# Optimization experiments

Measured on AMD Instinct MI355X. Metric: run time of the kernel, lower is better.

## Reference

```python
import jax, jax.numpy as jnp
import numpy as np

LAMBDA = 0.95   # fast-weight decay
ETA = 0.5       # Hebbian write rate
EPS = 1e-5      # LayerNorm epsilon
S_LOOP = 2      # inner read steps


def setup_inputs() -> dict:
    key = jax.random.key(0)
    ks = jax.random.split(key, 3)
    T, B, d_g, d_h = 32, 32, 256, 512
    z_seq = jax.random.normal(ks[0], (T, B, d_g), dtype=jnp.float32)
    # kaiming-uniform-ish / xavier-ish scaled weights
    W_h = jax.random.normal(ks[1], (d_h, d_h), dtype=jnp.float32) * (2.0 / d_h) ** 0.5
    W_g = jax.random.normal(ks[2], (d_h, d_g), dtype=jnp.float32) * (2.0 / (d_h + d_g)) ** 0.5
    b_h = jnp.zeros((d_h,), jnp.float32)
    ln_gamma = jnp.ones((d_h,), jnp.float32)
    ln_beta = jnp.zeros((d_h,), jnp.float32)
    return {"z_seq": z_seq, "W_h": W_h, "W_g": W_g, "b_h": b_h,
            "ln_gamma": ln_gamma, "ln_beta": ln_beta}


def reference(z_seq, W_h, W_g, b_h, ln_gamma, ln_beta):
    T, B, _ = z_seq.shape
    d_h = W_h.shape[0]

    def ln(x):
        mu = jnp.mean(x, axis=-1, keepdims=True)
        var = jnp.mean((x - mu) ** 2, axis=-1, keepdims=True)
        return (x - mu) * jax.lax.rsqrt(var + EPS) * ln_gamma + ln_beta

    def inner_read(h_base, A):
        # h = relu(LN(h_base)); then S fast-weight reads h <- relu(LN(h_base + A h))
        h = jax.nn.relu(ln(h_base))
        for _ in range(S_LOOP):
            Ah = jnp.einsum('bij,bj->bi', A, h)  # [B, d_h]
            h = jax.nn.relu(ln(h_base + Ah))
        return h

    def step(carry, z_t):
        h, A = carry
        h_base = h @ W_h.T + z_t @ W_g.T + b_h  # [B, d_h]
        h = inner_read(h_base, A)
        # Hebbian outer-product write: A <- lambda*A + eta * h h^T
        A = LAMBDA * A + ETA * jnp.einsum('bi,bj->bij', h, h)
        return (h, A), None

    h0 = jnp.zeros((B, d_h), z_seq.dtype)
    A0 = jnp.zeros((B, d_h, d_h), z_seq.dtype)
    (h, A), _ = jax.lax.scan(step, (h0, A0), z_seq[:-1])

    # last step: read-only (no A update)
    h_base = h @ W_h.T + z_seq[-1] @ W_g.T + b_h
    h = inner_read(h_base, A)
    return h
```

## Files before the change

### kernel.cpp

```cpp
#include <hip/hip_runtime.h>

typedef __attribute__((ext_vector_type(8))) short short8;
typedef __attribute__((ext_vector_type(4))) float f32x4;

constexpr int T_STEPS = 32;
constexpr int BATCH   = 32;
constexpr int DG      = 256;
constexpr int DH      = 512;
constexpr int NHIST   = 31;
constexpr int LDH     = 520;
constexpr int LDT     = 40;
constexpr float LAMBDA_ = 0.95f;
constexpr float ETA_    = 0.5f;
constexpr float EPS_    = 1e-5f;

__device__ __forceinline__ uint bf16cvt(float f) {
  uint u = __float_as_uint(f);
  return (u + 0x7FFFu + ((u >> 16) & 1u)) >> 16;
}
__device__ __forceinline__ uint pack2(float a, float b) {
  return bf16cvt(a) | (bf16cvt(b) << 16);
}

__global__ __launch_bounds__(512) void pack_kernel(
    const float* __restrict__ Wh, uint4* __restrict__ Wp) {
  const int f  = blockIdx.x * 512 + threadIdx.x;
  const int lf = f & 63;
  const int kk = (f >> 6) & 15;
  const int mt = f >> 10;
  const int r  = mt * 16 + (lf & 15);
  const int k0 = kk * 32 + (lf >> 4) * 8;
  const float4 a = *reinterpret_cast<const float4*>(Wh + (size_t)r * DH + k0);
  const float4 b = *reinterpret_cast<const float4*>(Wh + (size_t)r * DH + k0 + 4);
  Wp[f] = make_uint4(pack2(a.x, a.y), pack2(a.z, a.w),
                     pack2(b.x, b.y), pack2(b.z, b.w));
}

__global__ __launch_bounds__(512, 2) void rnn_kernel(
    const uint4* __restrict__ Wp, const float* __restrict__ z,
    const float* __restrict__ Wg, const float* __restrict__ bh,
    const float* __restrict__ g, const float* __restrict__ be,
    float* __restrict__ ZGg, float* __restrict__ out) {
  __shared__ uint4  stage[8][2][4][64];
  __shared__ ushort hist_bf[NHIST][LDH];
  __shared__ ushort histT[DH][LDT];
  __shared__ float  part[DH];
  __shared__ float  h_s[DH];
  __shared__ ushort hbf[DH];
  __shared__ float  red1[8], red2[8];
  __shared__ float  cc[NHIST + 1];
  __shared__ float  lam_pow[NHIST];

  const int tid  = threadIdx.x;
  const int lane = tid & 63;
  const int wave = tid >> 6;
  const int c    = lane & 15;
  const int gq   = lane >> 4;
  const int b    = blockIdx.x;
  const int r    = tid;

  if (tid == 0) {
    float p = 1.f;
    for (int k = 0; k < NHIST; ++k) { lam_pow[k] = p; p *= LAMBDA_; }
  }
  if (tid < NHIST + 1) cc[tid] = 0.f;
  {
    uint4 zz = make_uint4(0u, 0u, 0u, 0u);
#pragma unroll
    for (int i = 0; i < 5; ++i)
      reinterpret_cast<uint4*>(&histT[r][0])[i] = zz;
  }

  auto STAGE = [&](int kk, int slot) {
#pragma unroll
    for (int mt4 = 0; mt4 < 4; ++mt4) {
      const uint4* gsrc = Wp + (size_t)((wave * 4 + mt4) * 16 + kk) * 64 + lane;
      __builtin_amdgcn_global_load_lds(
          (const __attribute__((address_space(1))) uint*)gsrc,
          (__attribute__((address_space(3))) uint*)&stage[wave][slot][mt4][0],
          16, 0, 0);
    }
  };

#pragma unroll
  for (int mt4 = 0; mt4 < 4; ++mt4) {
    const int mt = wave * 4 + mt4;
    f32x4 acc0 = {0.f,0.f,0.f,0.f}, acc1 = {0.f,0.f,0.f,0.f};
#pragma unroll
    for (int kk = 0; kk < 8; ++kk) {
      const int k0 = kk * 32 + gq * 8;
      const float4 a  = *reinterpret_cast<const float4*>(Wg + (size_t)(mt*16 + c) * DG + k0);
      const float4 a2 = *reinterpret_cast<const float4*>(Wg + (size_t)(mt*16 + c) * DG + k0 + 4);
      const uint4 afu = make_uint4(pack2(a.x,a.y), pack2(a.z,a.w),
                                   pack2(a2.x,a2.y), pack2(a2.z,a2.w));
      const float* zb0 = z + ((size_t)c        * BATCH + b) * DG + k0;
      const float* zb1 = z + ((size_t)(16 + c) * BATCH + b) * DG + k0;
      const float4 b00 = *reinterpret_cast<const float4*>(zb0);
      const float4 b01 = *reinterpret_cast<const float4*>(zb0 + 4);
      const float4 b10 = *reinterpret_cast<const float4*>(zb1);
      const float4 b11 = *reinterpret_cast<const float4*>(zb1 + 4);
      const uint4 bf0 = make_uint4(pack2(b00.x,b00.y), pack2(b00.z,b00.w),
                                   pack2(b01.x,b01.y), pack2(b01.z,b01.w));
      const uint4 bf1 = make_uint4(pack2(b10.x,b10.y), pack2(b10.z,b10.w),
                                   pack2(b11.x,b11.y), pack2(b11.z,b11.w));
      acc0 = __builtin_amdgcn_mfma_f32_16x16x32_bf16(
          __builtin_bit_cast(short8, afu), __builtin_bit_cast(short8, bf0), acc0, 0,0,0);
      acc1 = __builtin_amdgcn_mfma_f32_16x16x32_bf16(
          __builtin_bit_cast(short8, afu), __builtin_bit_cast(short8, bf1), acc1, 0,0,0);
    }
    *reinterpret_cast<f32x4*>(&ZGg[((size_t)c        * BATCH + b) * DH + mt*16 + gq*4]) = acc0;
    *reinterpret_cast<f32x4*>(&ZGg[((size_t)(16 + c) * BATCH + b) * DH + mt*16 + gq*4]) = acc1;
  }
  __syncthreads();

  const float bh_r = bh[r], g_r = g[r], be_r = be[r];

  auto ln = [&](float x) -> float {
    float s1 = x, s2 = x * x;
#pragma unroll
    for (int off = 32; off; off >>= 1) {
      s1 += __shfl_xor(s1, off, 64);
      s2 += __shfl_xor(s2, off, 64);
    }
    if (lane == 0) { red1[wave] = s1; red2[wave] = s2; }
    __syncthreads();
    float a = 0.f, q = 0.f;
#pragma unroll
    for (int w2 = 0; w2 < 8; ++w2) { a += red1[w2]; q += red2[w2]; }
    const float mu = a * (1.f / DH);
    const float rs = rsqrtf(q * (1.f / DH) - mu * mu + EPS_);
    const float hv2 = fmaxf((x - mu) * rs * g_r + be_r, 0.f);
    h_s[r] = hv2;
    hbf[r] = (ushort)bf16cvt(hv2);
    __syncthreads();
    return hv2;
  };

  float hv = 0.f;
  for (int t = 0; t < T_STEPS; ++t) {
    float xb;
    if (t == 0) {
      xb = ZGg[(size_t)b * DH + r] + bh_r;
    } else {
      const float zgv = ZGg[((size_t)t * BATCH + b) * DH + r];
      asm volatile("s_waitcnt vmcnt(0)" ::: "memory");
      __builtin_amdgcn_sched_barrier(0);

      STAGE(0, 0);
      STAGE(1, 1);
      f32x4 acc[4] = {{0.f,0.f,0.f,0.f},{0.f,0.f,0.f,0.f},
                      {0.f,0.f,0.f,0.f},{0.f,0.f,0.f,0.f}};
#pragma unroll
      for (int kk = 0; kk < 16; ++kk) {
        const int slot = kk & 1;
        if (kk < 15) { asm volatile("s_waitcnt vmcnt(4)" ::: "memory"); }
        else         { asm volatile("s_waitcnt vmcnt(0)" ::: "memory"); }
        __builtin_amdgcn_sched_barrier(0);
        const uint4 a0 = stage[wave][slot][0][lane];
        const uint4 a1 = stage[wave][slot][1][lane];
        const uint4 a2 = stage[wave][slot][2][lane];
        const uint4 a3 = stage[wave][slot][3][lane];
        uint4 bvu = {0u,0u,0u,0u};
        if (c == 0)
          bvu = *reinterpret_cast<const uint4*>(&hbf[kk*32 + gq*8]);
        const short8 bv = __builtin_bit_cast(short8, bvu);
        acc[0] = __builtin_amdgcn_mfma_f32_16x16x32_bf16(
            __builtin_bit_cast(short8, a0), bv, acc[0], 0,0,0);
        acc[1] = __builtin_amdgcn_mfma_f32_16x16x32_bf16(
            __builtin_bit_cast(short8, a1), bv, acc[1], 0,0,0);
        acc[2] = __builtin_amdgcn_mfma_f32_16x16x32_bf16(
            __builtin_bit_cast(short8, a2), bv, acc[2], 0,0,0);
        acc[3] = __builtin_amdgcn_mfma_f32_16x16x32_bf16(
            __builtin_bit_cast(short8, a3), bv, acc[3], 0,0,0);
        if (kk < 14) STAGE(kk + 2, slot);
      }
      if (c == 0) {
#pragma unroll
        for (int mt4 = 0; mt4 < 4; ++mt4)
          *reinterpret_cast<f32x4*>(&part[(wave*4 + mt4)*16 + gq*4]) = acc[mt4];
      }
      __syncthreads();
      xb = part[r] + zgv + bh_r;
    }

    hv = ln(xb);

    if (t > 0) {
      for (int s = 0; s < 2; ++s) {
        const float4 c0 = *reinterpret_cast<const float4*>(&h_s[lane * 8]);
        const float4 c1 = *reinterpret_cast<const float4*>(&h_s[lane * 8 + 4]);
        for (int sp = wave; sp < t; sp += 8) {
          const uint4 hw = *reinterpret_cast<const uint4*>(&hist_bf[sp][lane * 8]);
          float d;
          d =      __uint_as_float(hw.x << 16)          * c0.x;
          d = fmaf(__uint_as_float(hw.x & 0xFFFF0000u), c0.y, d);
          d = fmaf(__uint_as_float(hw.y << 16),         c0.z, d);
          d = fmaf(__uint_as_float(hw.y & 0xFFFF0000u), c0.w, d);
          d = fmaf(__uint_as_float(hw.z << 16),         c1.x, d);
          d = fmaf(__uint_as_float(hw.z & 0xFFFF0000u), c1.y, d);
          d = fmaf(__uint_as_float(hw.w << 16),         c1.z, d);
          d = fmaf(__uint_as_float(hw.w & 0xFFFF0000u), c1.w, d);
#pragma unroll
          for (int off = 32; off; off >>= 1) d += __shfl_xor(d, off, 64);
          if (lane == 0) cc[sp] = ETA_ * lam_pow[t - 1 - sp] * d;
        }
        __syncthreads();
        float ah = 0.f;
#pragma unroll
        for (int q8 = 0; q8 < 4; ++q8) {
          const uint4 hw = *reinterpret_cast<const uint4*>(&histT[r][q8 * 8]);
          const uint w0 = hw.x, w1 = hw.y, w2 = hw.z, w3 = hw.w;
          ah = fmaf(cc[q8*8+0], __uint_as_float(w0 << 16),          ah);
          ah = fmaf(cc[q8*8+1], __uint_as_float(w0 & 0xFFFF0000u),  ah);
          ah = fmaf(cc[q8*8+2], __uint_as_float(w1 << 16),          ah);
          ah = fmaf(cc[q8*8+3], __uint_as_float(w1 & 0xFFFF0000u),  ah);
          ah = fmaf(cc[q8*8+4], __uint_as_float(w2 << 16),          ah);
          ah = fmaf(cc[q8*8+5], __uint_as_float(w2 & 0xFFFF0000u),  ah);
          ah = fmaf(cc[q8*8+6], __uint_as_float(w3 << 16),          ah);
          ah = fmaf(cc[q8*8+7], __uint_as_float(w3 & 0xFFFF0000u),  ah);
        }
        hv = ln(xb + ah);
      }
    }

    if (t < T_STEPS - 1) {
      const ushort hb16 = (ushort)bf16cvt(hv);
      hist_bf[t][r] = hb16;
      histT[r][t]   = hb16;
    }
  }

  out[(size_t)b * DH + r] = hv;
}

extern "C" void kernel_launch(void* const* d_in, const int* in_sizes, int n_in,
                              void* d_out, int out_size, void* d_ws, size_t ws_size,
                              hipStream_t stream) {
  const float* z     = (const float*)d_in[0];
  const float* W_h   = (const float*)d_in[1];
  const float* W_g   = (const float*)d_in[2];
  const float* b_h   = (const float*)d_in[3];
  const float* gamma = (const float*)d_in[4];
  const float* beta  = (const float*)d_in[5];
  float* out = (float*)d_out;

  float* ZGg = (float*)d_ws;
  uint4* Wp  = (uint4*)((char*)d_ws + (size_t)T_STEPS * BATCH * DH * 4);

  pack_kernel<<<dim3(64), dim3(512), 0, stream>>>(W_h, Wp);
  rnn_kernel<<<dim3(BATCH), dim3(512), 0, stream>>>(Wp, z, W_g, b_h,
                                                    gamma, beta, ZGg, out);
}
```

Measured before the change: 307.9 us.

## Compute fast-weight history dots with MFMA, keep ZG projection in LDS

Stores the Hebbian history in a single MFMA fragment layout in LDS. The history-times-h dot products now run as bf16 MFMAs with a cross-wave partial reduction, replacing per-wave shuffle reductions over two separate history copies. The precomputed input projection stays in LDS as bf16 instead of making a global round trip. The next step's W_h staging is prefetched across the step boundary, and __syncthreads is replaced by a lighter lgkmcnt-only barrier. In exchange the input projection loses precision to bf16, and the barrier no longer waits for outstanding global loads.

```diff
diff --git a/kernel.cpp b/kernel.cpp
--- a/kernel.cpp
+++ b/kernel.cpp
@@ -8,8 +8,6 @@
 constexpr int DG      = 256;
 constexpr int DH      = 512;
 constexpr int NHIST   = 31;
-constexpr int LDH     = 520;
-constexpr int LDT     = 40;
 constexpr float LAMBDA_ = 0.95f;
 constexpr float ETA_    = 0.5f;
 constexpr float EPS_    = 1e-5f;
@@ -20,6 +18,16 @@
 }
 __device__ __forceinline__ uint pack2(float a, float b) {
   return bf16cvt(a) | (bf16cvt(b) << 16);
+}
+__device__ __forceinline__ float bf2f(ushort u) {
+  return __uint_as_float(((uint)u) << 16);
+}
+
+__device__ __forceinline__ void block_barrier() {
+  __builtin_amdgcn_sched_barrier(0);
+  asm volatile("s_waitcnt lgkmcnt(0)" ::: "memory");
+  __builtin_amdgcn_s_barrier();
+  __builtin_amdgcn_sched_barrier(0);
 }
 
 __global__ __launch_bounds__(512) void pack_kernel(
@@ -40,15 +48,16 @@
     const uint4* __restrict__ Wp, const float* __restrict__ z,
     const float* __restrict__ Wg, const float* __restrict__ bh,
     const float* __restrict__ g, const float* __restrict__ be,
-    float* __restrict__ ZGg, float* __restrict__ out) {
+    float* __restrict__ out) {
   __shared__ uint4  stage[8][2][4][64];
-  __shared__ ushort hist_bf[NHIST][LDH];
-  __shared__ ushort histT[DH][LDT];
+  __shared__ uint4  hist_frag[2 * 16 * 64];
+  __shared__ ushort zg_bf[T_STEPS][DH];
   __shared__ float  part[DH];
   __shared__ float  h_s[DH];
   __shared__ ushort hbf[DH];
+  __shared__ float  pdots[8][32];
   __shared__ float  red1[8], red2[8];
-  __shared__ float  cc[NHIST + 1];
+  __shared__ float  cc[32];
   __shared__ float  lam_pow[NHIST];
 
   const int tid  = threadIdx.x;
@@ -63,13 +72,8 @@
     float p = 1.f;
     for (int k = 0; k < NHIST; ++k) { lam_pow[k] = p; p *= LAMBDA_; }
   }
-  if (tid < NHIST + 1) cc[tid] = 0.f;
-  {
-    uint4 zz = make_uint4(0u, 0u, 0u, 0u);
-#pragma unroll
-    for (int i = 0; i < 5; ++i)
-      reinterpret_cast<uint4*>(&histT[r][0])[i] = zz;
-  }
+  for (int i = tid; i < 2 * 16 * 64; i += 512)
+    hist_frag[i] = make_uint4(0u, 0u, 0u, 0u);
 
   auto STAGE = [&](int kk, int slot) {
 #pragma unroll
@@ -108,12 +112,15 @@
       acc1 = __builtin_amdgcn_mfma_f32_16x16x32_bf16(
           __builtin_bit_cast(short8, afu), __builtin_bit_cast(short8, bf1), acc1, 0,0,0);
     }
-    *reinterpret_cast<f32x4*>(&ZGg[((size_t)c        * BATCH + b) * DH + mt*16 + gq*4]) = acc0;
-    *reinterpret_cast<f32x4*>(&ZGg[((size_t)(16 + c) * BATCH + b) * DH + mt*16 + gq*4]) = acc1;
+    *reinterpret_cast<uint2*>(&zg_bf[c][mt*16 + gq*4]) =
+        make_uint2(pack2(acc0.x, acc0.y), pack2(acc0.z, acc0.w));
+    *reinterpret_cast<uint2*>(&zg_bf[16 + c][mt*16 + gq*4]) =
+        make_uint2(pack2(acc1.x, acc1.y), pack2(acc1.z, acc1.w));
   }
-  __syncthreads();
-
   const float bh_r = bh[r], g_r = g[r], be_r = be[r];
+  block_barrier();
+
+  STAGE(0, 0); STAGE(1, 1);
 
   auto ln = [&](float x) -> float {
     float s1 = x, s2 = x * x;
@@ -123,7 +130,7 @@
       s2 += __shfl_xor(s2, off, 64);
     }
     if (lane == 0) { red1[wave] = s1; red2[wave] = s2; }
-    __syncthreads();
+    block_barrier();
     float a = 0.f, q = 0.f;
 #pragma unroll
     for (int w2 = 0; w2 < 8; ++w2) { a += red1[w2]; q += red2[w2]; }
@@ -132,7 +139,7 @@
     const float hv2 = fmaxf((x - mu) * rs * g_r + be_r, 0.f);
     h_s[r] = hv2;
     hbf[r] = (ushort)bf16cvt(hv2);
-    __syncthreads();
+    block_barrier();
     return hv2;
   };
 
@@ -140,14 +147,8 @@
   for (int t = 0; t < T_STEPS; ++t) {
     float xb;
     if (t == 0) {
-      xb = ZGg[(size_t)b * DH + r] + bh_r;
+      xb = bf2f(zg_bf[0][r]) + bh_r;
     } else {
-      const float zgv = ZGg[((size_t)t * BATCH + b) * DH + r];
-      asm volatile("s_waitcnt vmcnt(0)" ::: "memory");
-      __builtin_amdgcn_sched_barrier(0);
-
-      STAGE(0, 0);
-      STAGE(1, 1);
       f32x4 acc[4] = {{0.f,0.f,0.f,0.f},{0.f,0.f,0.f,0.f},
                       {0.f,0.f,0.f,0.f},{0.f,0.f,0.f,0.f}};
 #pragma unroll
@@ -174,59 +175,66 @@
             __builtin_bit_cast(short8, a3), bv, acc[3], 0,0,0);
         if (kk < 14) STAGE(kk + 2, slot);
       }
+      if (t < T_STEPS - 1) { STAGE(0, 0); STAGE(1, 1); }
       if (c == 0) {
 #pragma unroll
         for (int mt4 = 0; mt4 < 4; ++mt4)
           *reinterpret_cast<f32x4*>(&part[(wave*4 + mt4)*16 + gq*4]) = acc[mt4];
       }
-      __syncthreads();
-      xb = part[r] + zgv + bh_r;
+      block_barrier();
+      xb = part[r] + bf2f(zg_bf[t][r]) + bh_r;
     }
 
     hv = ln(xb);
 
     if (t > 0) {
       for (int s = 0; s < 2; ++s) {
-        const float4 c0 = *reinterpret_cast<const float4*>(&h_s[lane * 8]);
-        const float4 c1 = *reinterpret_cast<const float4*>(&h_s[lane * 8 + 4]);
-        for (int sp = wave; sp < t; sp += 8) {
-          const uint4 hw = *reinterpret_cast<const uint4*>(&hist_bf[sp][lane * 8]);
-          float d;
-          d =      __uint_as_float(hw.x << 16)          * c0.x;
-          d = fmaf(__uint_as_float(hw.x & 0xFFFF0000u), c0.y, d);
-          d = fmaf(__uint_as_float(hw.y << 16),         c0.z, d);
-          d = fmaf(__uint_as_float(hw.y & 0xFFFF0000u), c0.w, d);
-          d = fmaf(__uint_as_float(hw.z << 16),         c1.x, d);
-          d = fmaf(__uint_as_float(hw.z & 0xFFFF0000u), c1.y, d);
-          d = fmaf(__uint_as_float(hw.w << 16),         c1.z, d);
-          d = fmaf(__uint_as_float(hw.w & 0xFFFF0000u), c1.w, d);
-#pragma unroll
-          for (int off = 32; off; off >>= 1) d += __shfl_xor(d, off, 64);
-          if (lane == 0) cc[sp] = ETA_ * lam_pow[t - 1 - sp] * d;
-        }
-        __syncthreads();
+        const int kk0 = 2 * wave, kk1 = kk0 + 1;
+        uint4 b0u = {0u,0u,0u,0u}, b1u = {0u,0u,0u,0u};
+        if (c == 0) {
+          b0u = *reinterpret_cast<const uint4*>(&hbf[kk0*32 + gq*8]);
+          b1u = *reinterpret_cast<const uint4*>(&hbf[kk1*32 + gq*8]);
+        }
+        const short8 b0 = __builtin_bit_cast(short8, b0u);
+        const short8 b1 = __builtin_bit_cast(short8, b1u);
+        f32x4 d0 = {0.f,0.f,0.f,0.f}, d1 = {0.f,0.f,0.f,0.f};
+        d0 = __builtin_amdgcn_mfma_f32_16x16x32_bf16(
+            __builtin_bit_cast(short8, hist_frag[kk0*64 + lane]), b0, d0, 0,0,0);
+        d0 = __builtin_amdgcn_mfma_f32_16x16x32_bf16(
+            __builtin_bit_cast(short8, hist_frag[kk1*64 + lane]), b1, d0, 0,0,0);
+        d1 = __builtin_amdgcn_mfma_f32_16x16x32_bf16(
+            __builtin_bit_cast(short8, hist_frag[(16+kk0)*64 + lane]), b0, d1, 0,0,0);
+        d1 = __builtin_amdgcn_mfma_f32_16x16x32_bf16(
+            __builtin_bit_cast(short8, hist_frag[(16+kk1)*64 + lane]), b1, d1, 0,0,0);
+        if (c == 0) {
+          *reinterpret_cast<f32x4*>(&pdots[wave][gq*4])      = d0;
+          *reinterpret_cast<f32x4*>(&pdots[wave][16 + gq*4]) = d1;
+        }
+        block_barrier();
+        if (tid < 32) {
+          float d = 0.f;
+#pragma unroll
+          for (int w = 0; w < 8; ++w) d += pdots[w][tid];
+          cc[tid] = (tid < t) ? ETA_ * lam_pow[t - 1 - tid] * d : 0.f;
+        }
+        block_barrier();
         float ah = 0.f;
-#pragma unroll
-        for (int q8 = 0; q8 < 4; ++q8) {
-          const uint4 hw = *reinterpret_cast<const uint4*>(&histT[r][q8 * 8]);
-          const uint w0 = hw.x, w1 = hw.y, w2 = hw.z, w3 = hw.w;
-          ah = fmaf(cc[q8*8+0], __uint_as_float(w0 << 16),          ah);
-          ah = fmaf(cc[q8*8+1], __uint_as_float(w0 & 0xFFFF0000u),  ah);
-          ah = fmaf(cc[q8*8+2], __uint_as_float(w1 << 16),          ah);
-          ah = fmaf(cc[q8*8+3], __uint_as_float(w1 & 0xFFFF0000u),  ah);
-          ah = fmaf(cc[q8*8+4], __uint_as_float(w2 << 16),          ah);
-          ah = fmaf(cc[q8*8+5], __uint_as_float(w2 & 0xFFFF0000u),  ah);
-          ah = fmaf(cc[q8*8+6], __uint_as_float(w3 << 16),          ah);
-          ah = fmaf(cc[q8*8+7], __uint_as_float(w3 & 0xFFFF0000u),  ah);
+        {
+          const ushort* hf = reinterpret_cast<const ushort*>(hist_frag);
+          const int base_r = ((r >> 5) * 64 + ((r >> 3) & 3) * 16) * 8 + (r & 7);
+#pragma unroll
+          for (int sp = 0; sp < NHIST; ++sp)
+            ah = fmaf(cc[sp], bf2f(hf[base_r + (sp & 15) * 8 + (sp >> 4) * 8192]), ah);
         }
         hv = ln(xb + ah);
       }
     }
 
     if (t < T_STEPS - 1) {
-      const ushort hb16 = (ushort)bf16cvt(hv);
-      hist_bf[t][r] = hb16;
-      histT[r][t]   = hb16;
+      ushort* hf = reinterpret_cast<ushort*>(hist_frag);
+      const int idx = (((t >> 4) * 16 + (r >> 5)) * 64 +
+                       ((r >> 3) & 3) * 16 + (t & 15)) * 8 + (r & 7);
+      hf[idx] = (ushort)bf16cvt(hv);
     }
   }
 
@@ -244,10 +252,9 @@
   const float* beta  = (const float*)d_in[5];
   float* out = (float*)d_out;
 
-  float* ZGg = (float*)d_ws;
-  uint4* Wp  = (uint4*)((char*)d_ws + (size_t)T_STEPS * BATCH * DH * 4);
+  uint4* Wp = (uint4*)d_ws;
 
   pack_kernel<<<dim3(64), dim3(512), 0, stream>>>(W_h, Wp);
   rnn_kernel<<<dim3(BATCH), dim3(512), 0, stream>>>(Wp, z, W_g, b_h,
-                                                    gamma, beta, ZGg, out);
-}
+                                                    gamma, beta, out);
+}
```

After: 320.9 us. 4.2% more time.

## Keep z·W_g projections in LDS as bf16 and pipeline W_h staging across steps

Applied to the files above, without the earlier changes.

The precomputed input projections z_t·W_g^T now stay in a shared bf16 buffer that doubles as the hidden-state history, so they no longer go to global workspace and get read back each step. W_h staging now runs continuously across timesteps, with wrap-around prefetch of the next step's first tiles instead of a full vmcnt(0) drain. The h operand is preloaded into registers in two halves rather than read per k-step. __syncthreads is replaced by a raw s_barrier with an lgkmcnt wait. The tradeoffs are extra bf16 rounding on the projection term and reliance on the LDS buffer being overwritten only after each slot is consumed.

```diff
diff --git a/kernel.cpp b/kernel.cpp
--- a/kernel.cpp
+++ b/kernel.cpp
@@ -8,8 +8,8 @@
 constexpr int DG      = 256;
 constexpr int DH      = 512;
 constexpr int NHIST   = 31;
-constexpr int LDH     = 520;
-constexpr int LDT     = 40;
+constexpr int LDH     = 528;
+constexpr int LDT     = 32;
 constexpr float LAMBDA_ = 0.95f;
 constexpr float ETA_    = 0.5f;
 constexpr float EPS_    = 1e-5f;
@@ -20,6 +20,16 @@
 }
 __device__ __forceinline__ uint pack2(float a, float b) {
   return bf16cvt(a) | (bf16cvt(b) << 16);
+}
+__device__ __forceinline__ float bf2f(ushort u) {
+  return __uint_as_float(((uint)u) << 16);
+}
+
+__device__ __forceinline__ void block_barrier() {
+  __builtin_amdgcn_sched_barrier(0);
+  asm volatile("s_waitcnt lgkmcnt(0)" ::: "memory");
+  __builtin_amdgcn_s_barrier();
+  __builtin_amdgcn_sched_barrier(0);
 }
 
 __global__ __launch_bounds__(512) void pack_kernel(
@@ -40,9 +50,9 @@
     const uint4* __restrict__ Wp, const float* __restrict__ z,
     const float* __restrict__ Wg, const float* __restrict__ bh,
     const float* __restrict__ g, const float* __restrict__ be,
-    float* __restrict__ ZGg, float* __restrict__ out) {
+    float* __restrict__ out) {
   __shared__ uint4  stage[8][2][4][64];
-  __shared__ ushort hist_bf[NHIST][LDH];
+  __shared__ ushort area_bf[T_STEPS][LDH];
   __shared__ ushort histT[DH][LDT];
   __shared__ float  part[DH];
   __shared__ float  h_s[DH];
@@ -67,7 +77,7 @@
   {
     uint4 zz = make_uint4(0u, 0u, 0u, 0u);
 #pragma unroll
-    for (int i = 0; i < 5; ++i)
+    for (int i = 0; i < 4; ++i)
       reinterpret_cast<uint4*>(&histT[r][0])[i] = zz;
   }
 
@@ -108,12 +118,15 @@
       acc1 = __builtin_amdgcn_mfma_f32_16x16x32_bf16(
           __builtin_bit_cast(short8, afu), __builtin_bit_cast(short8, bf1), acc1, 0,0,0);
     }
-    *reinterpret_cast<f32x4*>(&ZGg[((size_t)c        * BATCH + b) * DH + mt*16 + gq*4]) = acc0;
-    *reinterpret_cast<f32x4*>(&ZGg[((size_t)(16 + c) * BATCH + b) * DH + mt*16 + gq*4]) = acc1;
-  }
+    *reinterpret_cast<uint2*>(&area_bf[c][mt*16 + gq*4]) =
+        make_uint2(pack2(acc0.x, acc0.y), pack2(acc0.z, acc0.w));
+    *reinterpret_cast<uint2*>(&area_bf[16 + c][mt*16 + gq*4]) =
+        make_uint2(pack2(acc1.x, acc1.y), pack2(acc1.z, acc1.w));
+  }
+  const float bh_r = bh[r], g_r = g[r], be_r = be[r];
   __syncthreads();
 
-  const float bh_r = bh[r], g_r = g[r], be_r = be[r];
+  STAGE(0, 0); STAGE(1, 1);
 
   auto ln = [&](float x) -> float {
     float s1 = x, s2 = x * x;
@@ -123,7 +136,7 @@
       s2 += __shfl_xor(s2, off, 64);
     }
     if (lane == 0) { red1[wave] = s1; red2[wave] = s2; }
-    __syncthreads();
+    block_barrier();
     float a = 0.f, q = 0.f;
 #pragma unroll
     for (int w2 = 0; w2 < 8; ++w2) { a += red1[w2]; q += red2[w2]; }
@@ -132,7 +145,7 @@
     const float hv2 = fmaxf((x - mu) * rs * g_r + be_r, 0.f);
     h_s[r] = hv2;
     hbf[r] = (ushort)bf16cvt(hv2);
-    __syncthreads();
+    block_barrier();
     return hv2;
   };
 
@@ -140,30 +153,29 @@
   for (int t = 0; t < T_STEPS; ++t) {
     float xb;
     if (t == 0) {
-      xb = ZGg[(size_t)b * DH + r] + bh_r;
+      xb = bf2f(area_bf[0][r]) + bh_r;
     } else {
-      const float zgv = ZGg[((size_t)t * BATCH + b) * DH + r];
-      asm volatile("s_waitcnt vmcnt(0)" ::: "memory");
-      __builtin_amdgcn_sched_barrier(0);
-
-      STAGE(0, 0);
-      STAGE(1, 1);
       f32x4 acc[4] = {{0.f,0.f,0.f,0.f},{0.f,0.f,0.f,0.f},
                       {0.f,0.f,0.f,0.f},{0.f,0.f,0.f,0.f}};
+      uint4 bfr[8];
+#pragma unroll
+      for (int j = 0; j < 8; ++j)
+        bfr[j] = *reinterpret_cast<const uint4*>(&hbf[j*32 + gq*8]);
 #pragma unroll
       for (int kk = 0; kk < 16; ++kk) {
+        if (kk == 8) {
+#pragma unroll
+          for (int j = 0; j < 8; ++j)
+            bfr[j] = *reinterpret_cast<const uint4*>(&hbf[(j + 8)*32 + gq*8]);
+        }
+        asm volatile("s_waitcnt vmcnt(4)" ::: "memory");
+        __builtin_amdgcn_sched_barrier(0);
         const int slot = kk & 1;
-        if (kk < 15) { asm volatile("s_waitcnt vmcnt(4)" ::: "memory"); }
-        else         { asm volatile("s_waitcnt vmcnt(0)" ::: "memory"); }
-        __builtin_amdgcn_sched_barrier(0);
         const uint4 a0 = stage[wave][slot][0][lane];
         const uint4 a1 = stage[wave][slot][1][lane];
         const uint4 a2 = stage[wave][slot][2][lane];
         const uint4 a3 = stage[wave][slot][3][lane];
-        uint4 bvu = {0u,0u,0u,0u};
-        if (c == 0)
-          bvu = *reinterpret_cast<const uint4*>(&hbf[kk*32 + gq*8]);
-        const short8 bv = __builtin_bit_cast(short8, bvu);
+        const short8 bv = __builtin_bit_cast(short8, bfr[kk & 7]);
         acc[0] = __builtin_amdgcn_mfma_f32_16x16x32_bf16(
             __builtin_bit_cast(short8, a0), bv, acc[0], 0,0,0);
         acc[1] = __builtin_amdgcn_mfma_f32_16x16x32_bf16(
@@ -172,15 +184,15 @@
             __builtin_bit_cast(short8, a2), bv, acc[2], 0,0,0);
         acc[3] = __builtin_amdgcn_mfma_f32_16x16x32_bf16(
             __builtin_bit_cast(short8, a3), bv, acc[3], 0,0,0);
-        if (kk < 14) STAGE(kk + 2, slot);
+        STAGE((kk + 2) & 15, slot);
       }
       if (c == 0) {
 #pragma unroll
         for (int mt4 = 0; mt4 < 4; ++mt4)
           *reinterpret_cast<f32x4*>(&part[(wave*4 + mt4)*16 + gq*4]) = acc[mt4];
       }
-      __syncthreads();
-      xb = part[r] + zgv + bh_r;
+      block_barrier();
+      xb = part[r] + bf2f(area_bf[t][r]) + bh_r;
     }
 
     hv = ln(xb);
@@ -190,7 +202,7 @@
         const float4 c0 = *reinterpret_cast<const float4*>(&h_s[lane * 8]);
         const float4 c1 = *reinterpret_cast<const float4*>(&h_s[lane * 8 + 4]);
         for (int sp = wave; sp < t; sp += 8) {
-          const uint4 hw = *reinterpret_cast<const uint4*>(&hist_bf[sp][lane * 8]);
+          const uint4 hw = *reinterpret_cast<const uint4*>(&area_bf[sp][lane * 8]);
           float d;
           d =      __uint_as_float(hw.x << 16)          * c0.x;
           d = fmaf(__uint_as_float(hw.x & 0xFFFF0000u), c0.y, d);
@@ -204,7 +216,7 @@
           for (int off = 32; off; off >>= 1) d += __shfl_xor(d, off, 64);
           if (lane == 0) cc[sp] = ETA_ * lam_pow[t - 1 - sp] * d;
         }
-        __syncthreads();
+        block_barrier();
         float ah = 0.f;
 #pragma unroll
         for (int q8 = 0; q8 < 4; ++q8) {
@@ -224,9 +236,9 @@
     }
 
     if (t < T_STEPS - 1) {
-      const ushort hb16 = (ushort)bf16cvt(hv);
-      hist_bf[t][r] = hb16;
-      histT[r][t]   = hb16;
+      const ushort h16 = (ushort)bf16cvt(hv);
+      area_bf[t][r] = h16;
+      histT[r][t]   = h16;
     }
   }
 
@@ -244,10 +256,9 @@
   const float* beta  = (const float*)d_in[5];
   float* out = (float*)d_out;
 
-  float* ZGg = (float*)d_ws;
-  uint4* Wp  = (uint4*)((char*)d_ws + (size_t)T_STEPS * BATCH * DH * 4);
+  uint4* Wp = (uint4*)d_ws;
 
   pack_kernel<<<dim3(64), dim3(512), 0, stream>>>(W_h, Wp);
   rnn_kernel<<<dim3(BATCH), dim3(512), 0, stream>>>(Wp, z, W_g, b_h,
-                                                    gamma, beta, ZGg, out);
-}
+                                                    gamma, beta, out);
+}
```

After: 322.5 us. 1.05x slower.
